# Performance work log

Measured on AMD Instinct MI355X. Metric: run time of the kernel, lower is better.

Reference implementation:

```python
import jax, jax.numpy as jnp
import numpy as np

B, S, D, H = 2, 2048, 1024, 16
DK = D // H


def setup_inputs() -> dict:
    key = jax.random.key(0)
    ks = jax.random.split(key, 14)
    inp = {
        'query': jax.random.normal(ks[0], (B, S, D), jnp.float32),
        'key': jax.random.normal(ks[1], (B, S, D), jnp.float32),
        'value': jax.random.normal(ks[2], (B, S, D), jnp.float32),
        'mask': jax.random.randint(ks[3], (B, 1, S, S), 0, 2).astype(bool),
        'rel_pos_bias': jax.random.normal(ks[4], (1, H, S, S), jnp.float32),
    }
    scale = 1.0 / np.sqrt(D)
    names = ['Wq', 'bq', 'Wk', 'bk', 'Wv', 'bv', 'Wo', 'bo']
    for i, n in enumerate(names):
        k = ks[5 + i]
        if n.startswith('W'):
            inp[n] = jax.random.normal(k, (D, D), jnp.float32) * scale
        else:
            inp[n] = jnp.zeros((D,), jnp.float32)
    return inp


def reference(query, key, value, mask, rel_pos_bias, Wq, bq, Wk, bk, Wv, bv, Wo, bo):
    # torch Linear: y = x @ W^T + b; W stored [out, in]
    def proj(x, W, b):
        y = x @ W.T + b                       # [B,S,D]
        return y.reshape(B, S, H, DK).transpose(0, 2, 1, 3)  # [B,H,S,DK]

    q = proj(query, Wq, bq)
    k = proj(key, Wk, bk)
    v = proj(value, Wv, bv)

    scores = jnp.einsum('bhqd,bhkd->bhqk', q, k) / jnp.sqrt(jnp.float32(DK))
    scores = scores + rel_pos_bias
    scores = jnp.where(mask, jnp.float32(-1e9), scores)
    p_attn = jax.nn.softmax(scores, axis=-1)
    x = jnp.einsum('bhqk,bhkd->bhqd', p_attn, v)  # [B,H,S,DK]
    x = x.transpose(0, 2, 1, 3).reshape(B, S, D)
    return x @ Wo.T + bo
```

## Files before the change

### kernel.cpp

```cpp
#include <hip/hip_runtime.h>
#include <stdint.h>


typedef _Float16 f16;
typedef _Float16 f16x8 __attribute__((ext_vector_type(8)));
typedef _Float16 f16x4 __attribute__((ext_vector_type(4)));
typedef __fp16 h2 __attribute__((ext_vector_type(2)));
typedef float f32x4 __attribute__((ext_vector_type(4)));

#define LOG2E 1.44269504088896340736f

__device__ __forceinline__ void gload16(const void* g, void* l) {
  __builtin_amdgcn_global_load_lds(
      (const __attribute__((address_space(1))) unsigned int*)g,
      (__attribute__((address_space(3))) unsigned int*)l, 16, 0, 0);
}

struct CvtSrcs { const float* s[7]; };

__global__ __launch_bounds__(256) void cvt_all(CvtSrcs a, f16* __restrict__ out) {
  const int i = blockIdx.x * 256 + threadIdx.x;
  int r, base;
  if (i < 3145728) { r = i >> 20; base = r << 20; }
  else { r = 3 + ((i - 3145728) >> 18); base = 3145728 + ((r - 3) << 18); }
  const float4 v = ((const float4*)a.s[r])[i - base];
  f16x4 o = {(f16)v.x, (f16)v.y, (f16)v.z, (f16)v.w};
  ((f16x4*)out)[i] = o;
}

__global__ void mask_detect(const uint8_t* __restrict__ m, int* __restrict__ flag) {
  __shared__ int s_off, s_weird;
  const int t = threadIdx.x;
  if (t == 0) { s_off = 0; s_weird = 0; }
  __syncthreads();
  int f_off = 0, f_weird = 0;
  for (int i = t; i < 8192; i += 256) {
    const uint8_t v = m[i];
    if ((i & 3) && v) f_off = 1;
    if (v > 1) f_weird = 1;
  }
  if (f_off) atomicOr(&s_off, 1);
  if (f_weird) atomicOr(&s_weird, 1);
  __syncthreads();
  if (t == 0) *flag = (s_off && !s_weird) ? 1 : 0;
}

__global__ __launch_bounds__(256) void mask_canon(const uint8_t* __restrict__ m,
                                                  uint8_t* __restrict__ out,
                                                  const int* __restrict__ flag) {
  const int i = (blockIdx.x * 256 + threadIdx.x) * 4;
  uchar4 o;
  if (*flag) {
    const uchar4 v = *(const uchar4*)(m + i);
    o = make_uchar4(v.x != 0, v.y != 0, v.z != 0, v.w != 0);
  } else {
    const int4 v = *(const int4*)((const int*)m + i);
    o = make_uchar4(v.x != 0, v.y != 0, v.z != 0, v.w != 0);
  }
  *(uchar4*)(out + i) = o;
}

__global__ __launch_bounds__(256, 2) void gemm_qkv(
    const f16* __restrict__ qh, const f16* __restrict__ kh, const f16* __restrict__ vh,
    const f16* __restrict__ wq, const f16* __restrict__ wk, const f16* __restrict__ wv,
    const float* __restrict__ bq, const float* __restrict__ bk, const float* __restrict__ bv,
    f16* __restrict__ Qp, f16* __restrict__ Kp, f16* __restrict__ Vt) {
  constexpr int K = 1024;
  const int t = threadIdx.x;
  const int w = t >> 6, lane = t & 63, l15 = lane & 15, l4 = lane >> 4;
  const int nt = (int)blockIdx.x % 48;
  const int bm = ((int)blockIdx.x / 48) * 128;
  const int which = nt >> 4;
  const int bn = (nt & 15) * 64;
  const f16* A = which == 0 ? qh : which == 1 ? kh : vh;
  const f16* Bw = which == 0 ? wq : which == 1 ? wk : wv;
  const float* bias = which == 0 ? bq : which == 1 ? bk : bv;

  __shared__ f16 As[2][128 * 32];
  __shared__ f16 Bs[2][64 * 32];

  const f16* a0 = A + (size_t)(bm + (t >> 2)) * K + (t & 3) * 8;
  const f16* a1 = a0 + (size_t)64 * K;
  const f16* b0 = Bw + (size_t)(bn + (t >> 2)) * K + (t & 3) * 8;

  f32x4 acc[2][4];
#pragma unroll
  for (int m = 0; m < 2; ++m)
#pragma unroll
    for (int n = 0; n < 4; ++n) acc[m][n] = (f32x4){0.f, 0.f, 0.f, 0.f};

#define STAGE_G(buf, k0)                          \
  do {                                            \
    gload16(a0 + (k0), &As[buf][w * 512]);        \
    gload16(a1 + (k0), &As[buf][2048 + w * 512]); \
    gload16(b0 + (k0), &Bs[buf][w * 512]);        \
  } while (0)

  STAGE_G(0, 0);
  __syncthreads();
  int cur = 0;
#pragma unroll 1
  for (int kt = 0; kt < 32; ++kt) {
    if (kt < 31) STAGE_G(cur ^ 1, (kt + 1) * 32);
    const f16* ap = &As[cur][(w * 32 + l15) * 32 + l4 * 8];
    const f16* bp = &Bs[cur][l15 * 32 + l4 * 8];
    f16x8 af[2], bfr[4];
#pragma unroll
    for (int m = 0; m < 2; ++m) af[m] = *(const f16x8*)(ap + m * 512);
#pragma unroll
    for (int n = 0; n < 4; ++n) bfr[n] = *(const f16x8*)(bp + n * 512);
#pragma unroll
    for (int m = 0; m < 2; ++m)
#pragma unroll
      for (int n = 0; n < 4; ++n)
        acc[m][n] = __builtin_amdgcn_mfma_f32_16x16x32_f16(af[m], bfr[n], acc[m][n], 0, 0, 0);
    __syncthreads();
    cur ^= 1;
  }
#undef STAGE_G

  const float scale = which == 0 ? 0.125f * LOG2E : 1.0f;
  f16* outp = which == 0 ? Qp : which == 1 ? Kp : Vt;
#pragma unroll
  for (int m = 0; m < 2; ++m) {
    const int r0 = bm + w * 32 + m * 16 + (l4 << 2);
#pragma unroll
    for (int n = 0; n < 4; ++n) {
      const int c = bn + n * 16 + l15;
      const float bv = bias[c];
#pragma unroll
      for (int j = 0; j < 4; ++j) {
        const int r = r0 + j;
        const float v = (acc[m][n][j] + bv) * scale;
        const int b_ = r >> 11, s = r & 2047, h_ = c >> 6, dk = c & 63;
        if (which < 2)
          outp[(((size_t)b_ * 16 + h_) * 2048 + s) * 64 + dk] = (f16)v;
        else
          outp[(((size_t)b_ * 16 + h_) * 64 + dk) * 2048 + s] = (f16)v;
      }
    }
  }
}

__global__ __launch_bounds__(256, 2) void gemm_out(const f16* __restrict__ A,
                                                   const f16* __restrict__ Bw,
                                                   const float* __restrict__ bias,
                                                   float* __restrict__ outp) {
  constexpr int K = 1024;
  const int t = threadIdx.x;
  const int w = t >> 6, lane = t & 63, l15 = lane & 15, l4 = lane >> 4;
  const int bm = (int)(blockIdx.x >> 4) * 128;
  const int bn = (int)(blockIdx.x & 15) * 64;

  __shared__ f16 As[2][128 * 32];
  __shared__ f16 Bs[2][64 * 32];

  const f16* a0 = A + (size_t)(bm + (t >> 2)) * K + (t & 3) * 8;
  const f16* a1 = a0 + (size_t)64 * K;
  const f16* b0 = Bw + (size_t)(bn + (t >> 2)) * K + (t & 3) * 8;

  f32x4 acc[2][4];
#pragma unroll
  for (int m = 0; m < 2; ++m)
#pragma unroll
    for (int n = 0; n < 4; ++n) acc[m][n] = (f32x4){0.f, 0.f, 0.f, 0.f};

#define STAGE_G(buf, k0)                          \
  do {                                            \
    gload16(a0 + (k0), &As[buf][w * 512]);        \
    gload16(a1 + (k0), &As[buf][2048 + w * 512]); \
    gload16(b0 + (k0), &Bs[buf][w * 512]);        \
  } while (0)

  STAGE_G(0, 0);
  __syncthreads();
  int cur = 0;
#pragma unroll 1
  for (int kt = 0; kt < 32; ++kt) {
    if (kt < 31) STAGE_G(cur ^ 1, (kt + 1) * 32);
    const f16* ap = &As[cur][(w * 32 + l15) * 32 + l4 * 8];
    const f16* bp = &Bs[cur][l15 * 32 + l4 * 8];
    f16x8 af[2], bfr[4];
#pragma unroll
    for (int m = 0; m < 2; ++m) af[m] = *(const f16x8*)(ap + m * 512);
#pragma unroll
    for (int n = 0; n < 4; ++n) bfr[n] = *(const f16x8*)(bp + n * 512);
#pragma unroll
    for (int m = 0; m < 2; ++m)
#pragma unroll
      for (int n = 0; n < 4; ++n)
        acc[m][n] = __builtin_amdgcn_mfma_f32_16x16x32_f16(af[m], bfr[n], acc[m][n], 0, 0, 0);
    __syncthreads();
    cur ^= 1;
  }
#undef STAGE_G

#pragma unroll
  for (int m = 0; m < 2; ++m) {
    const int r0 = bm + w * 32 + m * 16 + (l4 << 2);
#pragma unroll
    for (int n = 0; n < 4; ++n) {
      const int c = bn + n * 16 + l15;
      const float bv = bias[c];
#pragma unroll
      for (int j = 0; j < 4; ++j)
        outp[(size_t)(r0 + j) * 1024 + c] = acc[m][n][j] + bv;
    }
  }
}

__device__ __forceinline__ const f16x8* swzr(const f16* base, int row, int bytecol) {
  return (const f16x8*)((const char*)base + row * 128 + (bytecol ^ ((row & 7) << 4)));
}

__global__ __launch_bounds__(256, 2) void attn_fwd(
    const f16* __restrict__ Qp, const f16* __restrict__ Kp,
    const f16* __restrict__ Vt, const float* __restrict__ bias,
    const uint8_t* __restrict__ mask, f16* __restrict__ X) {
  constexpr int S = 2048;
  const int bid = blockIdx.x;
  const int qt = bid & 31, h = bid >> 5;
  const int t = threadIdx.x, w = t >> 6, lane = t & 63;
  const int l15 = lane & 15, l4 = lane >> 4;
  const int q0 = qt * 64 + w * 16;

  const f16* Qb[2] = {Qp + (size_t)h * S * 64, Qp + (size_t)(16 + h) * S * 64};
  const f16* Kb[2] = {Kp + (size_t)h * S * 64, Kp + (size_t)(16 + h) * S * 64};
  const f16* Vb[2] = {Vt + (size_t)h * 64 * S, Vt + (size_t)(16 + h) * 64 * S};
  const float* biasr = bias + (size_t)h * S * S + (size_t)(q0 + l15) * S + l4 * 4;
  const uint8_t* mr0 = mask + (size_t)(q0 + l15) * S + l4 * 4;
  const uint8_t* mr1 = mr0 + (size_t)S * S;

  __shared__ f16 Ks[2][64 * 64];
  __shared__ f16 Vs[2][64 * 64];
  __shared__ f16 Ps[4][16 * 64];

  f16x8 qf[2][2];
#pragma unroll
  for (int bb = 0; bb < 2; ++bb)
#pragma unroll
    for (int ks = 0; ks < 2; ++ks)
      qf[bb][ks] =
          *(const f16x8*)(Qb[bb] + (size_t)(q0 + l15) * 64 + ks * 32 + l4 * 8);

  f32x4 oacc[2][4];
#pragma unroll
  for (int bb = 0; bb < 2; ++bb)
#pragma unroll
    for (int n = 0; n < 4; ++n) oacc[bb][n] = (f32x4){0.f, 0.f, 0.f, 0.f};
  float mrow[2] = {-3e38f, -3e38f}, lrow[2] = {0.f, 0.f};

  const int srow = t >> 3;
  const int scol = (((t & 7) ^ (srow & 7)) << 3);

#define STAGE(kk)                                                                   \
  do {                                                                              \
    gload16(Kb[0] + (size_t)((kk) + srow) * 64 + scol, &Ks[0][w * 512]);            \
    gload16(Kb[0] + (size_t)((kk) + 32 + srow) * 64 + scol, &Ks[0][2048 + w * 512]);\
    gload16(Kb[1] + (size_t)((kk) + srow) * 64 + scol, &Ks[1][w * 512]);            \
    gload16(Kb[1] + (size_t)((kk) + 32 + srow) * 64 + scol, &Ks[1][2048 + w * 512]);\
    gload16(Vb[0] + (size_t)srow * S + (kk) + scol, &Vs[0][w * 512]);               \
    gload16(Vb[0] + (size_t)(32 + srow) * S + (kk) + scol, &Vs[0][2048 + w * 512]); \
    gload16(Vb[1] + (size_t)srow * S + (kk) + scol, &Vs[1][w * 512]);               \
    gload16(Vb[1] + (size_t)(32 + srow) * S + (kk) + scol, &Vs[1][2048 + w * 512]); \
  } while (0)

  STAGE(0);

#pragma unroll 1
  for (int kt = 0; kt < 32; ++kt) {
    const int k0 = kt * 64;
    f32x4 bc[4];
    uint32_t mc[2][4];
#pragma unroll
    for (int n = 0; n < 4; ++n) {
      bc[n] = *(const f32x4*)(biasr + k0 + n * 16);
      mc[0][n] = *(const uint32_t*)(mr0 + k0 + n * 16);
      mc[1][n] = *(const uint32_t*)(mr1 + k0 + n * 16);
    }
    __syncthreads();

    f32x4 sacc[2][4];
#pragma unroll
    for (int bb = 0; bb < 2; ++bb)
#pragma unroll
      for (int n = 0; n < 4; ++n) sacc[bb][n] = (f32x4){0.f, 0.f, 0.f, 0.f};
#pragma unroll
    for (int bb = 0; bb < 2; ++bb)
#pragma unroll
      for (int n = 0; n < 4; ++n)
#pragma unroll
        for (int ks = 0; ks < 2; ++ks) {
          const f16x8 kf = *swzr(&Ks[bb][0], n * 16 + l15, ks * 64 + l4 * 16);
          sacc[bb][n] =
              __builtin_amdgcn_mfma_f32_16x16x32_f16(kf, qf[bb][ks], sacc[bb][n], 0, 0, 0);
        }

#pragma unroll
    for (int bb = 0; bb < 2; ++bb) {
      float tmax = -3e38f;
#pragma unroll
      for (int n = 0; n < 4; ++n) {
#pragma unroll
        for (int j = 0; j < 4; ++j) {
          const float mf = (float)((mc[bb][n] >> (8 * j)) & 255u);
          sacc[bb][n][j] = fmaf(mf, -2e9f, fmaf(bc[n][j], LOG2E, sacc[bb][n][j]));
        }
        tmax = fmaxf(tmax, fmaxf(fmaxf(sacc[bb][n][0], sacc[bb][n][1]),
                                 fmaxf(sacc[bb][n][2], sacc[bb][n][3])));
      }
      tmax = fmaxf(tmax, __shfl_xor(tmax, 16));
      tmax = fmaxf(tmax, __shfl_xor(tmax, 32));

      const float mnew = fmaxf(mrow[bb], tmax);
      const float alpha = __builtin_exp2f(mrow[bb] - mnew);
      mrow[bb] = mnew;
      float lsum = 0.f;
#pragma unroll
      for (int n = 0; n < 4; ++n)
#pragma unroll
        for (int j = 0; j < 4; ++j) {
          const float e = __builtin_exp2f(sacc[bb][n][j] - mnew);
          sacc[bb][n][j] = e;
          lsum += e;
        }
      lsum += __shfl_xor(lsum, 16);
      lsum += __shfl_xor(lsum, 32);
      lrow[bb] = lrow[bb] * alpha + lsum;

      float aq[4];
#pragma unroll
      for (int j = 0; j < 4; ++j) aq[j] = __shfl(alpha, l4 * 4 + j);
#pragma unroll
      for (int n = 0; n < 4; ++n)
#pragma unroll
        for (int j = 0; j < 4; ++j) oacc[bb][n][j] *= aq[j];

#pragma unroll
      for (int n = 0; n < 4; ++n) {
        h2 p01 = __builtin_amdgcn_cvt_pkrtz(sacc[bb][n][0], sacc[bb][n][1]);
        h2 p23 = __builtin_amdgcn_cvt_pkrtz(sacc[bb][n][2], sacc[bb][n][3]);
        f16x4 pk;
        pk[0] = (f16)p01[0]; pk[1] = (f16)p01[1];
        pk[2] = (f16)p23[0]; pk[3] = (f16)p23[1];
        *(f16x4*)((char*)&Ps[w][0] + l15 * 128 +
                  ((32 * n + 8 * l4) ^ ((l15 & 7) << 4))) = pk;
      }

      f16x8 pf[2];
#pragma unroll
      for (int ks = 0; ks < 2; ++ks)
        pf[ks] = *swzr(&Ps[w][0], l15, ks * 64 + l4 * 16);
#pragma unroll
      for (int ks = 0; ks < 2; ++ks)
#pragma unroll
        for (int n = 0; n < 4; ++n) {
          const f16x8 vf = *swzr(&Vs[bb][0], n * 16 + l15, ks * 64 + l4 * 16);
          oacc[bb][n] =
              __builtin_amdgcn_mfma_f32_16x16x32_f16(pf[ks], vf, oacc[bb][n], 0, 0, 0);
        }
    }

    __syncthreads();
    if (kt < 31) STAGE(k0 + 64);
  }
#undef STAGE

#pragma unroll
  for (int bb = 0; bb < 2; ++bb) {
    const float inv = 1.0f / lrow[bb];
    float invq[4];
#pragma unroll
    for (int j = 0; j < 4; ++j) invq[j] = __shfl(inv, l4 * 4 + j);
#pragma unroll
    for (int j = 0; j < 4; ++j) {
      const int qrow = q0 + l4 * 4 + j;
#pragma unroll
      for (int n = 0; n < 4; ++n)
        X[((size_t)bb * 2048 + qrow) * 1024 + h * 64 + n * 16 + l15] =
            (f16)(oacc[bb][n][j] * invq[j]);
    }
  }
}

extern "C" void kernel_launch(void* const* d_in, const int* in_sizes, int n_in,
                              void* d_out, int out_size, void* d_ws, size_t ws_size,
                              hipStream_t stream) {
  const float* query = (const float*)d_in[0];
  const float* key_ = (const float*)d_in[1];
  const float* value = (const float*)d_in[2];
  const uint8_t* mask = (const uint8_t*)d_in[3];
  const float* bias = (const float*)d_in[4];
  const float* Wq = (const float*)d_in[5];
  const float* bq = (const float*)d_in[6];
  const float* Wk = (const float*)d_in[7];
  const float* bk = (const float*)d_in[8];
  const float* Wv = (const float*)d_in[9];
  const float* bv = (const float*)d_in[10];
  const float* Wo = (const float*)d_in[11];
  const float* bo = (const float*)d_in[12];

  char* p = (char*)d_ws;
  f16* qh = (f16*)p; p += (size_t)4194304 * 2;
  f16* kh = (f16*)p; p += (size_t)4194304 * 2;
  f16* vh = (f16*)p; p += (size_t)4194304 * 2;
  f16* wqh = (f16*)p; p += (size_t)1048576 * 2;
  f16* wkh = (f16*)p; p += (size_t)1048576 * 2;
  f16* wvh = (f16*)p; p += (size_t)1048576 * 2;
  f16* woh = (f16*)p; p += (size_t)1048576 * 2;
  f16* Qp = (f16*)p; p += (size_t)4194304 * 2;
  f16* Kp = (f16*)p; p += (size_t)4194304 * 2;
  f16* Vt = (f16*)p; p += (size_t)4194304 * 2;
  f16* Xh = (f16*)p; p += (size_t)4194304 * 2;
  uint8_t* m8 = (uint8_t*)p; p += (size_t)8388608;
  int* flag = (int*)p; p += 256;
  if (ws_size < (size_t)(p - (char*)d_ws)) return;

  mask_detect<<<1, 256, 0, stream>>>(mask, flag);
  mask_canon<<<8192, 256, 0, stream>>>(mask, m8, flag);

  CvtSrcs cs;
  cs.s[0] = query; cs.s[1] = key_; cs.s[2] = value;
  cs.s[3] = Wq; cs.s[4] = Wk; cs.s[5] = Wv; cs.s[6] = Wo;
  cvt_all<<<16384, 256, 0, stream>>>(cs, qh);

  gemm_qkv<<<1536, 256, 0, stream>>>(qh, kh, vh, wqh, wkh, wvh, bq, bk, bv,
                                     Qp, Kp, Vt);

  attn_fwd<<<512, 256, 0, stream>>>(Qp, Kp, Vt, bias, m8, Xh);

  gemm_out<<<512, 256, 0, stream>>>(Xh, woh, bo, (float*)d_out);
}
```

Baseline: 256.6 us.

## Double-buffer K/V and bias/mask loads with two-tile-ahead prefetch in attention

Expands the K/V shared-memory tiles to two buffers and keeps bias/mask register sets for two tiles, prefetching two tiles ahead and waiting on a partial vmcnt so global loads overlap compute. It also remaps block IDs so consecutive blocks go to different heads/query tiles, which may change L2 locality across XCDs. The last iterations issue wrapped-around redundant loads, and the extra LDS and registers may reduce occupancy.

```diff
diff --git a/kernel.cpp b/kernel.cpp
--- a/kernel.cpp
+++ b/kernel.cpp
@@ -219,7 +219,8 @@
     const uint8_t* __restrict__ mask, f16* __restrict__ X) {
   constexpr int S = 2048;
   const int bid = blockIdx.x;
-  const int qt = bid & 31, h = bid >> 5;
+  const int sb = (bid & 7) * 64 + (bid >> 3);
+  const int qt = sb & 31, h = sb >> 5;
   const int t = threadIdx.x, w = t >> 6, lane = t & 63;
   const int l15 = lane & 15, l4 = lane >> 4;
   const int q0 = qt * 64 + w * 16;
@@ -231,8 +232,8 @@
   const uint8_t* mr0 = mask + (size_t)(q0 + l15) * S + l4 * 4;
   const uint8_t* mr1 = mr0 + (size_t)S * S;
 
-  __shared__ f16 Ks[2][64 * 64];
-  __shared__ f16 Vs[2][64 * 64];
+  __shared__ f16 Ks[2][2][64 * 64];
+  __shared__ f16 Vs[2][2][64 * 64];
   __shared__ f16 Ps[4][16 * 64];
 
   f16x8 qf[2][2];
@@ -250,121 +251,126 @@
     for (int n = 0; n < 4; ++n) oacc[bb][n] = (f32x4){0.f, 0.f, 0.f, 0.f};
   float mrow[2] = {-3e38f, -3e38f}, lrow[2] = {0.f, 0.f};
 
+  f32x4 bc[2][4];
+  uint32_t mc[2][2][4];
+
   const int srow = t >> 3;
   const int scol = (((t & 7) ^ (srow & 7)) << 3);
 
-#define STAGE(kk)                                                                   \
-  do {                                                                              \
-    gload16(Kb[0] + (size_t)((kk) + srow) * 64 + scol, &Ks[0][w * 512]);            \
-    gload16(Kb[0] + (size_t)((kk) + 32 + srow) * 64 + scol, &Ks[0][2048 + w * 512]);\
-    gload16(Kb[1] + (size_t)((kk) + srow) * 64 + scol, &Ks[1][w * 512]);            \
-    gload16(Kb[1] + (size_t)((kk) + 32 + srow) * 64 + scol, &Ks[1][2048 + w * 512]);\
-    gload16(Vb[0] + (size_t)srow * S + (kk) + scol, &Vs[0][w * 512]);               \
-    gload16(Vb[0] + (size_t)(32 + srow) * S + (kk) + scol, &Vs[0][2048 + w * 512]); \
-    gload16(Vb[1] + (size_t)srow * S + (kk) + scol, &Vs[1][w * 512]);               \
-    gload16(Vb[1] + (size_t)(32 + srow) * S + (kk) + scol, &Vs[1][2048 + w * 512]); \
+#define STAGE(bf, kk)                                                                    \
+  do {                                                                                   \
+    gload16(Kb[0] + (size_t)((kk) + srow) * 64 + scol, &Ks[bf][0][w * 512]);             \
+    gload16(Kb[0] + (size_t)((kk) + 32 + srow) * 64 + scol, &Ks[bf][0][2048 + w * 512]); \
+    gload16(Kb[1] + (size_t)((kk) + srow) * 64 + scol, &Ks[bf][1][w * 512]);             \
+    gload16(Kb[1] + (size_t)((kk) + 32 + srow) * 64 + scol, &Ks[bf][1][2048 + w * 512]); \
+    gload16(Vb[0] + (size_t)srow * S + (kk) + scol, &Vs[bf][0][w * 512]);                \
+    gload16(Vb[0] + (size_t)(32 + srow) * S + (kk) + scol, &Vs[bf][0][2048 + w * 512]);  \
+    gload16(Vb[1] + (size_t)srow * S + (kk) + scol, &Vs[bf][1][w * 512]);                \
+    gload16(Vb[1] + (size_t)(32 + srow) * S + (kk) + scol, &Vs[bf][1][2048 + w * 512]);  \
   } while (0)
 
-  STAGE(0);
+#define LOADB(SET, kk)                                      \
+  do {                                                      \
+    bc[SET][0] = *(const f32x4*)(biasr + (kk));             \
+    bc[SET][1] = *(const f32x4*)(biasr + (kk) + 16);        \
+    bc[SET][2] = *(const f32x4*)(biasr + (kk) + 32);        \
+    bc[SET][3] = *(const f32x4*)(biasr + (kk) + 48);        \
+    mc[SET][0][0] = *(const uint32_t*)(mr0 + (kk));         \
+    mc[SET][0][1] = *(const uint32_t*)(mr0 + (kk) + 16);    \
+    mc[SET][0][2] = *(const uint32_t*)(mr0 + (kk) + 32);    \
+    mc[SET][0][3] = *(const uint32_t*)(mr0 + (kk) + 48);    \
+    mc[SET][1][0] = *(const uint32_t*)(mr1 + (kk));         \
+    mc[SET][1][1] = *(const uint32_t*)(mr1 + (kk) + 16);    \
+    mc[SET][1][2] = *(const uint32_t*)(mr1 + (kk) + 32);    \
+    mc[SET][1][3] = *(const uint32_t*)(mr1 + (kk) + 48);    \
+  } while (0)
+
+#define TILE(BUF, SET, KNEXT)                                                            \
+  do {                                                                                   \
+    asm volatile("s_waitcnt vmcnt(20)" ::: "memory");                                    \
+    __builtin_amdgcn_s_barrier();                                                        \
+    asm volatile("" ::: "memory");                                                       \
+    f32x4 sacc[2][4];                                                                    \
+    _Pragma("unroll") for (int bb = 0; bb < 2; ++bb)                                     \
+      _Pragma("unroll") for (int n = 0; n < 4; ++n)                                      \
+        sacc[bb][n] = (f32x4){0.f, 0.f, 0.f, 0.f};                                       \
+    _Pragma("unroll") for (int bb = 0; bb < 2; ++bb)                                     \
+      _Pragma("unroll") for (int n = 0; n < 4; ++n)                                      \
+        _Pragma("unroll") for (int ks = 0; ks < 2; ++ks) {                               \
+          const f16x8 kf = *swzr(&Ks[BUF][bb][0], n * 16 + l15, ks * 64 + l4 * 16);      \
+          sacc[bb][n] = __builtin_amdgcn_mfma_f32_16x16x32_f16(kf, qf[bb][ks],           \
+                                                               sacc[bb][n], 0, 0, 0);    \
+        }                                                                                \
+    _Pragma("unroll") for (int bb = 0; bb < 2; ++bb) {                                   \
+      float tmax = -3e38f;                                                               \
+      _Pragma("unroll") for (int n = 0; n < 4; ++n) {                                    \
+        _Pragma("unroll") for (int j = 0; j < 4; ++j) {                                  \
+          const float mf = (float)((mc[SET][bb][n] >> (8 * j)) & 255u);                  \
+          sacc[bb][n][j] =                                                               \
+              fmaf(mf, -2e9f, fmaf(bc[SET][n][j], LOG2E, sacc[bb][n][j]));               \
+        }                                                                                \
+        tmax = fmaxf(tmax, fmaxf(fmaxf(sacc[bb][n][0], sacc[bb][n][1]),                  \
+                                 fmaxf(sacc[bb][n][2], sacc[bb][n][3])));                \
+      }                                                                                  \
+      tmax = fmaxf(tmax, __shfl_xor(tmax, 16));                                          \
+      tmax = fmaxf(tmax, __shfl_xor(tmax, 32));                                          \
+      const float mnew = fmaxf(mrow[bb], tmax);                                          \
+      const float alpha = __builtin_exp2f(mrow[bb] - mnew);                              \
+      mrow[bb] = mnew;                                                                   \
+      float lsum = 0.f;                                                                  \
+      _Pragma("unroll") for (int n = 0; n < 4; ++n)                                      \
+        _Pragma("unroll") for (int j = 0; j < 4; ++j) {                                  \
+          const float e = __builtin_exp2f(sacc[bb][n][j] - mnew);                        \
+          sacc[bb][n][j] = e;                                                            \
+          lsum += e;                                                                     \
+        }                                                                                \
+      lsum += __shfl_xor(lsum, 16);                                                      \
+      lsum += __shfl_xor(lsum, 32);                                                      \
+      lrow[bb] = lrow[bb] * alpha + lsum;                                                \
+      float aq[4];                                                                       \
+      _Pragma("unroll") for (int j = 0; j < 4; ++j) aq[j] = __shfl(alpha, l4 * 4 + j);   \
+      _Pragma("unroll") for (int n = 0; n < 4; ++n)                                      \
+        _Pragma("unroll") for (int j = 0; j < 4; ++j) oacc[bb][n][j] *= aq[j];           \
+      _Pragma("unroll") for (int n = 0; n < 4; ++n) {                                    \
+        h2 p01 = __builtin_amdgcn_cvt_pkrtz(sacc[bb][n][0], sacc[bb][n][1]);             \
+        h2 p23 = __builtin_amdgcn_cvt_pkrtz(sacc[bb][n][2], sacc[bb][n][3]);             \
+        f16x4 pk;                                                                        \
+        pk[0] = (f16)p01[0]; pk[1] = (f16)p01[1];                                        \
+        pk[2] = (f16)p23[0]; pk[3] = (f16)p23[1];                                        \
+        *(f16x4*)((char*)&Ps[w][0] + l15 * 128 +                                         \
+                  ((32 * n + 8 * l4) ^ ((l15 & 7) << 4))) = pk;                          \
+      }                                                                                  \
+      f16x8 pf[2];                                                                       \
+      _Pragma("unroll") for (int ks = 0; ks < 2; ++ks)                                   \
+        pf[ks] = *swzr(&Ps[w][0], l15, ks * 64 + l4 * 16);                               \
+      _Pragma("unroll") for (int ks = 0; ks < 2; ++ks)                                   \
+        _Pragma("unroll") for (int n = 0; n < 4; ++n) {                                  \
+          const f16x8 vf = *swzr(&Vs[BUF][bb][0], n * 16 + l15, ks * 64 + l4 * 16);      \
+          oacc[bb][n] = __builtin_amdgcn_mfma_f32_16x16x32_f16(pf[ks], vf,               \
+                                                               oacc[bb][n], 0, 0, 0);    \
+        }                                                                                \
+    }                                                                                    \
+    __builtin_amdgcn_s_barrier();                                                        \
+    asm volatile("" ::: "memory");                                                       \
+    STAGE(BUF, KNEXT);                                                                   \
+    LOADB(SET, KNEXT);                                                                   \
+  } while (0)
+
+  STAGE(0, 0);
+  LOADB(0, 0);
+  STAGE(1, 64);
+  LOADB(1, 64);
 
 #pragma unroll 1
-  for (int kt = 0; kt < 32; ++kt) {
-    const int k0 = kt * 64;
-    f32x4 bc[4];
-    uint32_t mc[2][4];
-#pragma unroll
-    for (int n = 0; n < 4; ++n) {
-      bc[n] = *(const f32x4*)(biasr + k0 + n * 16);
-      mc[0][n] = *(const uint32_t*)(mr0 + k0 + n * 16);
-      mc[1][n] = *(const uint32_t*)(mr1 + k0 + n * 16);
-    }
-    __syncthreads();
-
-    f32x4 sacc[2][4];
-#pragma unroll
-    for (int bb = 0; bb < 2; ++bb)
-#pragma unroll
-      for (int n = 0; n < 4; ++n) sacc[bb][n] = (f32x4){0.f, 0.f, 0.f, 0.f};
-#pragma unroll
-    for (int bb = 0; bb < 2; ++bb)
-#pragma unroll
-      for (int n = 0; n < 4; ++n)
-#pragma unroll
-        for (int ks = 0; ks < 2; ++ks) {
-          const f16x8 kf = *swzr(&Ks[bb][0], n * 16 + l15, ks * 64 + l4 * 16);
-          sacc[bb][n] =
-              __builtin_amdgcn_mfma_f32_16x16x32_f16(kf, qf[bb][ks], sacc[bb][n], 0, 0, 0);
-        }
-
-#pragma unroll
-    for (int bb = 0; bb < 2; ++bb) {
-      float tmax = -3e38f;
-#pragma unroll
-      for (int n = 0; n < 4; ++n) {
-#pragma unroll
-        for (int j = 0; j < 4; ++j) {
-          const float mf = (float)((mc[bb][n] >> (8 * j)) & 255u);
-          sacc[bb][n][j] = fmaf(mf, -2e9f, fmaf(bc[n][j], LOG2E, sacc[bb][n][j]));
-        }
-        tmax = fmaxf(tmax, fmaxf(fmaxf(sacc[bb][n][0], sacc[bb][n][1]),
-                                 fmaxf(sacc[bb][n][2], sacc[bb][n][3])));
-      }
-      tmax = fmaxf(tmax, __shfl_xor(tmax, 16));
-      tmax = fmaxf(tmax, __shfl_xor(tmax, 32));
-
-      const float mnew = fmaxf(mrow[bb], tmax);
-      const float alpha = __builtin_exp2f(mrow[bb] - mnew);
-      mrow[bb] = mnew;
-      float lsum = 0.f;
-#pragma unroll
-      for (int n = 0; n < 4; ++n)
-#pragma unroll
-        for (int j = 0; j < 4; ++j) {
-          const float e = __builtin_exp2f(sacc[bb][n][j] - mnew);
-          sacc[bb][n][j] = e;
-          lsum += e;
-        }
-      lsum += __shfl_xor(lsum, 16);
-      lsum += __shfl_xor(lsum, 32);
-      lrow[bb] = lrow[bb] * alpha + lsum;
-
-      float aq[4];
-#pragma unroll
-      for (int j = 0; j < 4; ++j) aq[j] = __shfl(alpha, l4 * 4 + j);
-#pragma unroll
-      for (int n = 0; n < 4; ++n)
-#pragma unroll
-        for (int j = 0; j < 4; ++j) oacc[bb][n][j] *= aq[j];
-
-#pragma unroll
-      for (int n = 0; n < 4; ++n) {
-        h2 p01 = __builtin_amdgcn_cvt_pkrtz(sacc[bb][n][0], sacc[bb][n][1]);
-        h2 p23 = __builtin_amdgcn_cvt_pkrtz(sacc[bb][n][2], sacc[bb][n][3]);
-        f16x4 pk;
-        pk[0] = (f16)p01[0]; pk[1] = (f16)p01[1];
-        pk[2] = (f16)p23[0]; pk[3] = (f16)p23[1];
-        *(f16x4*)((char*)&Ps[w][0] + l15 * 128 +
-                  ((32 * n + 8 * l4) ^ ((l15 & 7) << 4))) = pk;
-      }
-
-      f16x8 pf[2];
-#pragma unroll
-      for (int ks = 0; ks < 2; ++ks)
-        pf[ks] = *swzr(&Ps[w][0], l15, ks * 64 + l4 * 16);
-#pragma unroll
-      for (int ks = 0; ks < 2; ++ks)
-#pragma unroll
-        for (int n = 0; n < 4; ++n) {
-          const f16x8 vf = *swzr(&Vs[bb][0], n * 16 + l15, ks * 64 + l4 * 16);
-          oacc[bb][n] =
-              __builtin_amdgcn_mfma_f32_16x16x32_f16(pf[ks], vf, oacc[bb][n], 0, 0, 0);
-        }
-    }
-
-    __syncthreads();
-    if (kt < 31) STAGE(k0 + 64);
-  }
+  for (int kt = 0; kt < 32; kt += 2) {
+    TILE(0, 0, ((kt + 2) * 64) & (S - 1));
+    TILE(1, 1, ((kt + 3) * 64) & (S - 1));
+  }
+#undef TILE
+#undef LOADB
 #undef STAGE
+
+  asm volatile("s_waitcnt vmcnt(0)" ::: "memory");
 
 #pragma unroll
   for (int bb = 0; bb < 2; ++bb) {
```

Measured after the change: 273.0 us. 1.06x slower.
